# Kernel tuning notes

Measured on AMD Instinct MI355X. Metric: run time of the kernel, lower is better.

## Reference

```python
import jax, jax.numpy as jnp
import numpy as np

HIDDEN = 1024
NUM_HEADS = 16
HEAD_DIM = HIDDEN // NUM_HEADS


def setup_inputs() -> dict:
    key = jax.random.key(0)
    ks = jax.random.split(key, 9)
    B, S, Hs = 2, 2048, HIDDEN
    scale = 1.0 / np.sqrt(Hs)
    inp = {
        "hidden_state": jax.random.normal(ks[0], (B, S, Hs), dtype=jnp.float32),
        # causal mask, exactly (B, num_heads, S, S) as the module's assert requires
        "attention_mask": jnp.broadcast_to(
            jnp.tril(jnp.ones((S, S), dtype=bool)), (B, NUM_HEADS, S, S)
        ),
        "wq": jax.random.normal(ks[1], (Hs, Hs), dtype=jnp.float32) * scale,
        "bq": jnp.zeros((Hs,), dtype=jnp.float32),
        "wk": jax.random.normal(ks[2], (Hs, Hs), dtype=jnp.float32) * scale,
        "bk": jnp.zeros((Hs,), dtype=jnp.float32),
        "wv": jax.random.normal(ks[3], (Hs, Hs), dtype=jnp.float32) * scale,
        "bv": jnp.zeros((Hs,), dtype=jnp.float32),
        "wo": jax.random.normal(ks[4], (Hs, Hs), dtype=jnp.float32) * scale,
        "bo": jnp.zeros((Hs,), dtype=jnp.float32),
    }
    return inp


def _split_heads(x):
    B, S, _ = x.shape
    return x.reshape(B, S, NUM_HEADS, HEAD_DIM).transpose(0, 2, 1, 3)  # (B,H,S,D)


def reference(hidden_state, attention_mask, wq, bq, wk, bk, wv, bv, wo, bo):
    B, S, Hs = hidden_state.shape
    # torch nn.Linear: x @ W.T + b
    q = _split_heads(hidden_state @ wq.T + bq)
    k = _split_heads(hidden_state @ wk.T + bk)
    v = _split_heads(hidden_state @ wv.T + bv)
    scores = jnp.einsum("bhsd,bhtd->bhst", q, k) / jnp.sqrt(
        jnp.asarray(HEAD_DIM, dtype=jnp.float32)
    )
    scores = jnp.where(attention_mask, scores, -jnp.inf)
    probs = jax.nn.softmax(scores, axis=-1)
    # dropout p=0.0 (eval/deterministic) -> identity
    out = jnp.einsum("bhst,bhtd->bhsd", probs, v)
    out = out.transpose(0, 2, 1, 3).reshape(B, S, Hs)
    return out @ wo.T + bo
```

## Files before the change

kernel.cpp:

```cpp
#include <hip/hip_runtime.h>
#include <stdint.h>
#include <stddef.h>


typedef __attribute__((ext_vector_type(8))) short short8;
typedef __attribute__((ext_vector_type(4))) float f32x4;
typedef __attribute__((ext_vector_type(4))) unsigned int u32x4;
typedef __attribute__((ext_vector_type(4))) unsigned short u16x4;

static __device__ __forceinline__ unsigned short f2bf(float f){
  union { float f; unsigned u; } v; v.f = f;
  unsigned r = v.u + 0x7FFFu + ((v.u >> 16) & 1u);
  return (unsigned short)(r >> 16);
}

static __device__ __forceinline__ void gl_lds16(const void* g, void* l){
  __builtin_amdgcn_global_load_lds((const __attribute__((address_space(1))) void*)g,
                                   (__attribute__((address_space(3))) void*)l, 16, 0, 0);
}

__global__ __launch_bounds__(256) void k_cvt_all(const float* __restrict__ X,
                                                 const float* __restrict__ w0, const float* __restrict__ w1,
                                                 const float* __restrict__ w2, const float* __restrict__ w3,
                                                 unsigned short* __restrict__ Xb,
                                                 unsigned short* __restrict__ Wb){
  int bid = blockIdx.x;
  const float* src; unsigned short* dst; int i;
  if (bid < 4096){ src = X; dst = Xb; i = bid*256 + threadIdx.x; }
  else {
    int w = (bid - 4096) >> 10;
    const float* srcs[4] = {w0,w1,w2,w3};
    src = srcs[w]; dst = Wb + (size_t)w*1048576u;
    i = ((bid - 4096) & 1023)*256 + threadIdx.x;
  }
  f32x4 x = ((const f32x4*)src)[i];
  u16x4 y = { f2bf(x[0]), f2bf(x[1]), f2bf(x[2]), f2bf(x[3]) };
  ((u16x4*)dst)[i] = y;
}

template<int MODE>
__global__ __launch_bounds__(256) void k_gemm_bt(
    const unsigned short* __restrict__ A,
    const unsigned short* __restrict__ B,
    const float* __restrict__ bias0, const float* __restrict__ bias1, const float* __restrict__ bias2,
    void* __restrict__ Cout, int N, int K)
{
  __shared__ unsigned short lds_a[128*32];
  __shared__ unsigned short lds_b[128*32];
  const int t = threadIdx.x;
  const int lane = t & 63, wave = t >> 6;
  const int wy = wave >> 1, wx = wave & 1;
  const int m0 = blockIdx.y * 128, n0 = blockIdx.x * 128;
  const int mrow = lane & 15, quad = lane >> 4;
  const unsigned short* ga = A + (size_t)(m0 + (t>>2)) * K + (t&3)*8;
  const unsigned short* gb = B + (size_t)(n0 + (t>>2)) * K + (t&3)*8;
  char* la = (char*)lds_a + wave*1024;
  char* lb = (char*)lds_b + wave*1024;

  f32x4 acc[4][4];
  #pragma unroll
  for (int i=0;i<4;i++)
    #pragma unroll
    for (int j=0;j<4;j++) acc[i][j] = (f32x4){0.f,0.f,0.f,0.f};

  for (int k0=0;k0<K;k0+=32){
    __syncthreads();
    #pragma unroll
    for (int p=0;p<2;p++){
      gl_lds16(ga + (size_t)p*64*K + k0, la + p*4096);
      gl_lds16(gb + (size_t)p*64*K + k0, lb + p*4096);
    }
    __syncthreads();
    short8 af[4], bf[4];
    #pragma unroll
    for (int i=0;i<4;i++) af[i] = *(const short8*)(lds_a + (wy*64+i*16+mrow)*32 + quad*8);
    #pragma unroll
    for (int j=0;j<4;j++) bf[j] = *(const short8*)(lds_b + (wx*64+j*16+mrow)*32 + quad*8);
    #pragma unroll
    for (int i=0;i<4;i++)
      #pragma unroll
      for (int j=0;j<4;j++)
        acc[i][j] = __builtin_amdgcn_mfma_f32_16x16x32_bf16(af[i], bf[j], acc[i][j], 0,0,0);
  }

  #pragma unroll
  for (int j=0;j<4;j++){
    int col = n0 + wx*64 + j*16 + mrow;
    float bv;
    if (MODE==0){
      int cb = col >> 10;
      const float* bp = (cb==0)?bias0:((cb==1)?bias1:bias2);
      bv = bp[col & 1023];
    } else {
      bv = bias0[col];
    }
    #pragma unroll
    for (int i=0;i<4;i++){
      int rbase = m0 + wy*64 + i*16 + quad*4;
      #pragma unroll
      for (int r=0;r<4;r++){
        float v = acc[i][j][r] + bv;
        if (MODE==1) ((float*)Cout)[(size_t)(rbase+r)*N + col] = v;
        else         ((unsigned short*)Cout)[(size_t)(rbase+r)*N + col] = f2bf(v);
      }
    }
  }
}

__global__ __launch_bounds__(256) void k_vt(const unsigned short* __restrict__ QKV,
                                            unsigned short* __restrict__ Vt){
  __shared__ unsigned short tile[64][72];
  const int bh = blockIdx.y, b = bh >> 4, h = bh & 15;
  const int s0 = blockIdx.x * 64;
  const unsigned short* vp = QKV + (size_t)b*2048*3072 + 2048 + (size_t)h*64;
  const int r = threadIdx.x >> 3, c = (threadIdx.x & 7) * 8;
  #pragma unroll
  for (int p=0;p<2;p++){
    int s = r + p*32;
    *(u32x4*)&tile[s][c] = *(const u32x4*)(vp + (size_t)(s0+s)*3072 + c);
  }
  __syncthreads();
  unsigned short* op = Vt + (size_t)bh*64*2048;
  #pragma unroll
  for (int p=0;p<2;p++){
    int d = r + p*32;
    union { short8 v; unsigned short u[8]; } o;
    #pragma unroll
    for (int i=0;i<8;i++) o.u[i] = tile[c+i][d];
    *(short8*)(op + (size_t)d*2048 + s0 + c) = o.v;
  }
}

__global__ __launch_bounds__(256) void k_attn(const unsigned short* __restrict__ QKV,
                                              const unsigned short* __restrict__ Vt,
                                              unsigned short* __restrict__ Ctx){
  __shared__ unsigned short lds_k[64*72];
  __shared__ unsigned short lds_v[64*72];
  __shared__ unsigned short lds_p[4][16*72];
  const int t = threadIdx.x;
  const int lane = t & 63, wave = t >> 6;
  const int mrow = lane & 15, quad = lane >> 4;
  const int bh = blockIdx.y, b = bh >> 4, h = bh & 15;
  const int q0 = blockIdx.x * 64;
  const size_t qkvbase = (size_t)b*2048*3072 + (size_t)h*64;

  short8 qf[2];
  {
    const unsigned short* qp = QKV + qkvbase + (size_t)(q0 + wave*16 + mrow) * 3072;
    qf[0] = *(const short8*)(qp + quad*8);
    qf[1] = *(const short8*)(qp + 32 + quad*8);
  }
  float m_i[4], l_i[4]; f32x4 oacc[4];
  #pragma unroll
  for (int r=0;r<4;r++){ m_i[r] = -1e30f; l_i[r] = 0.f; }
  #pragma unroll
  for (int c=0;c<4;c++) oacc[c] = (f32x4){0.f,0.f,0.f,0.f};

  const int grow0 = q0 + wave*16 + quad*4;
  const int njt = blockIdx.x + 1;
  const unsigned short* kbase = QKV + qkvbase + 1024;
  const unsigned short* vbase = Vt + (size_t)bh*64*2048;
  const int sr = t >> 3, sc = (t & 7) * 8;

  for (int jt=0;jt<njt;jt++){
    const int j0 = jt*64;
    __syncthreads();
    #pragma unroll
    for (int p=0;p<2;p++){
      int r = sr + p*32;
      *(u32x4*)(lds_k + r*72 + sc) = *(const u32x4*)(kbase + (size_t)(j0+r)*3072 + sc);
      *(u32x4*)(lds_v + r*72 + sc) = *(const u32x4*)(vbase + (size_t)r*2048 + j0 + sc);
    }
    __syncthreads();

    f32x4 sacc[4];
    #pragma unroll
    for (int jj=0;jj<4;jj++) sacc[jj] = (f32x4){0.f,0.f,0.f,0.f};
    #pragma unroll
    for (int jj=0;jj<4;jj++)
      #pragma unroll
      for (int kk=0;kk<2;kk++){
        short8 kf = *(const short8*)(lds_k + (jj*16+mrow)*72 + kk*32 + quad*8);
        sacc[jj] = __builtin_amdgcn_mfma_f32_16x16x32_bf16(qf[kk], kf, sacc[jj], 0,0,0);
      }

    float s[4][4];
    if (jt == njt-1){
      #pragma unroll
      for (int jj=0;jj<4;jj++){
        int gcol = j0 + jj*16 + mrow;
        #pragma unroll
        for (int r=0;r<4;r++){
          float v = sacc[jj][r] * 0.125f;
          s[jj][r] = (gcol <= grow0 + r) ? v : -1e30f;
        }
      }
    } else {
      #pragma unroll
      for (int jj=0;jj<4;jj++)
        #pragma unroll
        for (int r=0;r<4;r++) s[jj][r] = sacc[jj][r] * 0.125f;
    }

    float alpha[4];
    #pragma unroll
    for (int r=0;r<4;r++){
      float v = fmaxf(fmaxf(s[0][r],s[1][r]), fmaxf(s[2][r],s[3][r]));
      #pragma unroll
      for (int off=1;off<16;off<<=1) v = fmaxf(v, __shfl_xor(v, off));
      float mn = fmaxf(m_i[r], v);
      alpha[r] = __expf(m_i[r] - mn);
      m_i[r] = mn;
    }
    #pragma unroll
    for (int r=0;r<4;r++){
      float sum = 0.f;
      #pragma unroll
      for (int jj=0;jj<4;jj++){
        float p = __expf(s[jj][r] - m_i[r]);
        s[jj][r] = p; sum += p;
      }
      #pragma unroll
      for (int off=1;off<16;off<<=1) sum += __shfl_xor(sum, off);
      l_i[r] = l_i[r]*alpha[r] + sum;
    }
    #pragma unroll
    for (int c=0;c<4;c++)
      #pragma unroll
      for (int r=0;r<4;r++) oacc[c][r] *= alpha[r];

    unsigned short* pp = lds_p[wave];
    #pragma unroll
    for (int jj=0;jj<4;jj++)
      #pragma unroll
      for (int r=0;r<4;r++)
        pp[(quad*4+r)*72 + jj*16 + mrow] = f2bf(s[jj][r]);
    __asm__ volatile("s_waitcnt lgkmcnt(0)" ::: "memory");
    short8 pf[2];
    pf[0] = *(const short8*)(pp + mrow*72 + quad*8);
    pf[1] = *(const short8*)(pp + mrow*72 + 32 + quad*8);

    #pragma unroll
    for (int c=0;c<4;c++)
      #pragma unroll
      for (int kk=0;kk<2;kk++){
        short8 vf = *(const short8*)(lds_v + (c*16+mrow)*72 + kk*32 + quad*8);
        oacc[c] = __builtin_amdgcn_mfma_f32_16x16x32_bf16(pf[kk], vf, oacc[c], 0,0,0);
      }
  }

  unsigned short* cp = Ctx + (size_t)b*2048*1024 + (size_t)h*64;
  #pragma unroll
  for (int c=0;c<4;c++)
    #pragma unroll
    for (int r=0;r<4;r++){
      float v = oacc[c][r] / l_i[r];
      cp[(size_t)(q0 + wave*16 + quad*4 + r)*1024 + c*16 + mrow] = f2bf(v);
    }
}

extern "C" void kernel_launch(void* const* d_in, const int* in_sizes, int n_in,
                              void* d_out, int out_size, void* d_ws, size_t ws_size,
                              hipStream_t stream){
  const float* X  = (const float*)d_in[0];
  const float* wq = (const float*)d_in[2];
  const float* bq = (const float*)d_in[3];
  const float* wk = (const float*)d_in[4];
  const float* bk = (const float*)d_in[5];
  const float* wv = (const float*)d_in[6];
  const float* bv = (const float*)d_in[7];
  const float* wo = (const float*)d_in[8];
  const float* bo = (const float*)d_in[9];

  char* ws = (char*)d_ws;
  unsigned short* Xb   = (unsigned short*)(ws);
  unsigned short* Wb   = (unsigned short*)(ws + (8u<<20));
  unsigned short* QKVb = (unsigned short*)(ws + (16u<<20));
  unsigned short* Vt   = (unsigned short*)(ws + (40u<<20));
  unsigned short* Ctxb = (unsigned short*)(ws + (48u<<20));

  k_cvt_all<<<dim3(8192), 256, 0, stream>>>(X, wq, wk, wv, wo, Xb, Wb);
  k_gemm_bt<0><<<dim3(24, 32), 256, 0, stream>>>(Xb, Wb, bq, bk, bv, QKVb, 3072, 1024);
  k_vt  <<<dim3(32, 32), 256, 0, stream>>>(QKVb, Vt);
  k_attn<<<dim3(32, 32), 256, 0, stream>>>(QKVb, Vt, Ctxb);
  k_gemm_bt<1><<<dim3(8, 32), 256, 0, stream>>>(Ctxb, Wb + 3u*1048576u, bo, bo, bo,
                                                d_out, 1024, 1024);
}
```

Measured before the change: 795.3 us.

## Process two query tiles per attention block and use 64-row tiles for output GEMM

The attention kernel now handles 128 query rows per block as two 64-row halves that share each loaded K/V tile. This halves K/V global traffic per query, and the first half skips the final diagonal tile. The output projection GEMM gets a 64-row M-tile variant with twice as many blocks, to fill more CUs on the small 1024-wide GEMM. The cost is fewer attention blocks (512), more registers per thread, and possible load imbalance from the causal triangle.

```diff
diff --git a/kernel.cpp b/kernel.cpp
--- a/kernel.cpp
+++ b/kernel.cpp
@@ -38,46 +38,48 @@
   ((u16x4*)dst)[i] = y;
 }
 
-template<int MODE>
+template<int MODE, int MT>
 __global__ __launch_bounds__(256) void k_gemm_bt(
     const unsigned short* __restrict__ A,
     const unsigned short* __restrict__ B,
     const float* __restrict__ bias0, const float* __restrict__ bias1, const float* __restrict__ bias2,
     void* __restrict__ Cout, int N, int K)
 {
-  __shared__ unsigned short lds_a[128*32];
+  static_assert(MT==64 || MT==128, "MT");
+  constexpr int I  = MT/32;
+  constexpr int NA = MT/64;
+  __shared__ unsigned short lds_a[MT*32];
   __shared__ unsigned short lds_b[128*32];
   const int t = threadIdx.x;
   const int lane = t & 63, wave = t >> 6;
   const int wy = wave >> 1, wx = wave & 1;
-  const int m0 = blockIdx.y * 128, n0 = blockIdx.x * 128;
+  const int m0 = blockIdx.y * MT, n0 = blockIdx.x * 128;
   const int mrow = lane & 15, quad = lane >> 4;
   const unsigned short* ga = A + (size_t)(m0 + (t>>2)) * K + (t&3)*8;
   const unsigned short* gb = B + (size_t)(n0 + (t>>2)) * K + (t&3)*8;
   char* la = (char*)lds_a + wave*1024;
   char* lb = (char*)lds_b + wave*1024;
 
-  f32x4 acc[4][4];
-  #pragma unroll
-  for (int i=0;i<4;i++)
+  f32x4 acc[I][4];
+  #pragma unroll
+  for (int i=0;i<I;i++)
     #pragma unroll
     for (int j=0;j<4;j++) acc[i][j] = (f32x4){0.f,0.f,0.f,0.f};
 
   for (int k0=0;k0<K;k0+=32){
     __syncthreads();
     #pragma unroll
-    for (int p=0;p<2;p++){
-      gl_lds16(ga + (size_t)p*64*K + k0, la + p*4096);
-      gl_lds16(gb + (size_t)p*64*K + k0, lb + p*4096);
-    }
+    for (int p=0;p<NA;p++) gl_lds16(ga + (size_t)p*64*K + k0, la + p*4096);
+    #pragma unroll
+    for (int p=0;p<2;p++)  gl_lds16(gb + (size_t)p*64*K + k0, lb + p*4096);
     __syncthreads();
-    short8 af[4], bf[4];
-    #pragma unroll
-    for (int i=0;i<4;i++) af[i] = *(const short8*)(lds_a + (wy*64+i*16+mrow)*32 + quad*8);
+    short8 af[I], bf[4];
+    #pragma unroll
+    for (int i=0;i<I;i++) af[i] = *(const short8*)(lds_a + (wy*(MT/2)+i*16+mrow)*32 + quad*8);
     #pragma unroll
     for (int j=0;j<4;j++) bf[j] = *(const short8*)(lds_b + (wx*64+j*16+mrow)*32 + quad*8);
     #pragma unroll
-    for (int i=0;i<4;i++)
+    for (int i=0;i<I;i++)
       #pragma unroll
       for (int j=0;j<4;j++)
         acc[i][j] = __builtin_amdgcn_mfma_f32_16x16x32_bf16(af[i], bf[j], acc[i][j], 0,0,0);
@@ -95,8 +97,8 @@
       bv = bias0[col];
     }
     #pragma unroll
-    for (int i=0;i<4;i++){
-      int rbase = m0 + wy*64 + i*16 + quad*4;
+    for (int i=0;i<I;i++){
+      int rbase = m0 + wy*(MT/2) + i*16 + quad*4;
       #pragma unroll
       for (int r=0;r<4;r++){
         float v = acc[i][j][r] + bv;
@@ -141,23 +143,26 @@
   const int lane = t & 63, wave = t >> 6;
   const int mrow = lane & 15, quad = lane >> 4;
   const int bh = blockIdx.y, b = bh >> 4, h = bh & 15;
-  const int q0 = blockIdx.x * 64;
+  const int q0 = blockIdx.x * 128;
   const size_t qkvbase = (size_t)b*2048*3072 + (size_t)h*64;
 
-  short8 qf[2];
-  {
-    const unsigned short* qp = QKV + qkvbase + (size_t)(q0 + wave*16 + mrow) * 3072;
-    qf[0] = *(const short8*)(qp + quad*8);
-    qf[1] = *(const short8*)(qp + 32 + quad*8);
-  }
-  float m_i[4], l_i[4]; f32x4 oacc[4];
-  #pragma unroll
-  for (int r=0;r<4;r++){ m_i[r] = -1e30f; l_i[r] = 0.f; }
-  #pragma unroll
-  for (int c=0;c<4;c++) oacc[c] = (f32x4){0.f,0.f,0.f,0.f};
-
-  const int grow0 = q0 + wave*16 + quad*4;
-  const int njt = blockIdx.x + 1;
+  short8 qf[2][2];
+  #pragma unroll
+  for (int qh=0;qh<2;qh++){
+    const unsigned short* qp = QKV + qkvbase + (size_t)(q0 + qh*64 + wave*16 + mrow) * 3072;
+    qf[qh][0] = *(const short8*)(qp + quad*8);
+    qf[qh][1] = *(const short8*)(qp + 32 + quad*8);
+  }
+  float m_i[2][4], l_i[2][4]; f32x4 oacc[2][4];
+  #pragma unroll
+  for (int qh=0;qh<2;qh++){
+    #pragma unroll
+    for (int r=0;r<4;r++){ m_i[qh][r] = -1e30f; l_i[qh][r] = 0.f; }
+    #pragma unroll
+    for (int c=0;c<4;c++) oacc[qh][c] = (f32x4){0.f,0.f,0.f,0.f};
+  }
+
+  const int njt = 2*blockIdx.x + 2;
   const unsigned short* kbase = QKV + qkvbase + 1024;
   const unsigned short* vbase = Vt + (size_t)bh*64*2048;
   const int sr = t >> 3, sc = (t & 7) * 8;
@@ -173,90 +178,98 @@
     }
     __syncthreads();
 
-    f32x4 sacc[4];
-    #pragma unroll
-    for (int jj=0;jj<4;jj++) sacc[jj] = (f32x4){0.f,0.f,0.f,0.f};
-    #pragma unroll
-    for (int jj=0;jj<4;jj++)
-      #pragma unroll
-      for (int kk=0;kk<2;kk++){
-        short8 kf = *(const short8*)(lds_k + (jj*16+mrow)*72 + kk*32 + quad*8);
-        sacc[jj] = __builtin_amdgcn_mfma_f32_16x16x32_bf16(qf[kk], kf, sacc[jj], 0,0,0);
-      }
-
-    float s[4][4];
-    if (jt == njt-1){
-      #pragma unroll
-      for (int jj=0;jj<4;jj++){
-        int gcol = j0 + jj*16 + mrow;
-        #pragma unroll
-        for (int r=0;r<4;r++){
-          float v = sacc[jj][r] * 0.125f;
-          s[jj][r] = (gcol <= grow0 + r) ? v : -1e30f;
+    #pragma unroll
+    for (int qh=0;qh<2;qh++){
+      if (qh==0 && jt==njt-1) continue;
+      const int grow0 = q0 + qh*64 + wave*16 + quad*4;
+
+      f32x4 sacc[4];
+      #pragma unroll
+      for (int jj=0;jj<4;jj++) sacc[jj] = (f32x4){0.f,0.f,0.f,0.f};
+      #pragma unroll
+      for (int jj=0;jj<4;jj++)
+        #pragma unroll
+        for (int kk=0;kk<2;kk++){
+          short8 kf = *(const short8*)(lds_k + (jj*16+mrow)*72 + kk*32 + quad*8);
+          sacc[jj] = __builtin_amdgcn_mfma_f32_16x16x32_bf16(qf[qh][kk], kf, sacc[jj], 0,0,0);
         }
-      }
-    } else {
+
+      float s[4][4];
+      if (jt == 2*blockIdx.x + qh){
+        #pragma unroll
+        for (int jj=0;jj<4;jj++){
+          int gcol = j0 + jj*16 + mrow;
+          #pragma unroll
+          for (int r=0;r<4;r++){
+            float v = sacc[jj][r] * 0.125f;
+            s[jj][r] = (gcol <= grow0 + r) ? v : -1e30f;
+          }
+        }
+      } else {
+        #pragma unroll
+        for (int jj=0;jj<4;jj++)
+          #pragma unroll
+          for (int r=0;r<4;r++) s[jj][r] = sacc[jj][r] * 0.125f;
+      }
+
+      float alpha[4];
+      #pragma unroll
+      for (int r=0;r<4;r++){
+        float v = fmaxf(fmaxf(s[0][r],s[1][r]), fmaxf(s[2][r],s[3][r]));
+        #pragma unroll
+        for (int off=1;off<16;off<<=1) v = fmaxf(v, __shfl_xor(v, off));
+        float mn = fmaxf(m_i[qh][r], v);
+        alpha[r] = __expf(m_i[qh][r] - mn);
+        m_i[qh][r] = mn;
+      }
+      #pragma unroll
+      for (int r=0;r<4;r++){
+        float sum = 0.f;
+        #pragma unroll
+        for (int jj=0;jj<4;jj++){
+          float p = __expf(s[jj][r] - m_i[qh][r]);
+          s[jj][r] = p; sum += p;
+        }
+        #pragma unroll
+        for (int off=1;off<16;off<<=1) sum += __shfl_xor(sum, off);
+        l_i[qh][r] = l_i[qh][r]*alpha[r] + sum;
+      }
+      #pragma unroll
+      for (int c=0;c<4;c++)
+        #pragma unroll
+        for (int r=0;r<4;r++) oacc[qh][c][r] *= alpha[r];
+
+      unsigned short* pp = lds_p[wave];
       #pragma unroll
       for (int jj=0;jj<4;jj++)
         #pragma unroll
-        for (int r=0;r<4;r++) s[jj][r] = sacc[jj][r] * 0.125f;
+        for (int r=0;r<4;r++)
+          pp[(quad*4+r)*72 + jj*16 + mrow] = f2bf(s[jj][r]);
+      __asm__ volatile("s_waitcnt lgkmcnt(0)" ::: "memory");
+      short8 pf[2];
+      pf[0] = *(const short8*)(pp + mrow*72 + quad*8);
+      pf[1] = *(const short8*)(pp + mrow*72 + 32 + quad*8);
+
+      #pragma unroll
+      for (int c=0;c<4;c++)
+        #pragma unroll
+        for (int kk=0;kk<2;kk++){
+          short8 vf = *(const short8*)(lds_v + (c*16+mrow)*72 + kk*32 + quad*8);
+          oacc[qh][c] = __builtin_amdgcn_mfma_f32_16x16x32_bf16(pf[kk], vf, oacc[qh][c], 0,0,0);
+        }
     }
-
-    float alpha[4];
-    #pragma unroll
-    for (int r=0;r<4;r++){
-      float v = fmaxf(fmaxf(s[0][r],s[1][r]), fmaxf(s[2][r],s[3][r]));
-      #pragma unroll
-      for (int off=1;off<16;off<<=1) v = fmaxf(v, __shfl_xor(v, off));
-      float mn = fmaxf(m_i[r], v);
-      alpha[r] = __expf(m_i[r] - mn);
-      m_i[r] = mn;
-    }
-    #pragma unroll
-    for (int r=0;r<4;r++){
-      float sum = 0.f;
-      #pragma unroll
-      for (int jj=0;jj<4;jj++){
-        float p = __expf(s[jj][r] - m_i[r]);
-        s[jj][r] = p; sum += p;
-      }
-      #pragma unroll
-      for (int off=1;off<16;off<<=1) sum += __shfl_xor(sum, off);
-      l_i[r] = l_i[r]*alpha[r] + sum;
-    }
+  }
+
+  unsigned short* cp = Ctx + (size_t)b*2048*1024 + (size_t)h*64;
+  #pragma unroll
+  for (int qh=0;qh<2;qh++)
     #pragma unroll
     for (int c=0;c<4;c++)
       #pragma unroll
-      for (int r=0;r<4;r++) oacc[c][r] *= alpha[r];
-
-    unsigned short* pp = lds_p[wave];
-    #pragma unroll
-    for (int jj=0;jj<4;jj++)
-      #pragma unroll
-      for (int r=0;r<4;r++)
-        pp[(quad*4+r)*72 + jj*16 + mrow] = f2bf(s[jj][r]);
-    __asm__ volatile("s_waitcnt lgkmcnt(0)" ::: "memory");
-    short8 pf[2];
-    pf[0] = *(const short8*)(pp + mrow*72 + quad*8);
-    pf[1] = *(const short8*)(pp + mrow*72 + 32 + quad*8);
-
-    #pragma unroll
-    for (int c=0;c<4;c++)
-      #pragma unroll
-      for (int kk=0;kk<2;kk++){
-        short8 vf = *(const short8*)(lds_v + (c*16+mrow)*72 + kk*32 + quad*8);
-        oacc[c] = __builtin_amdgcn_mfma_f32_16x16x32_bf16(pf[kk], vf, oacc[c], 0,0,0);
-      }
-  }
-
-  unsigned short* cp = Ctx + (size_t)b*2048*1024 + (size_t)h*64;
-  #pragma unroll
-  for (int c=0;c<4;c++)
-    #pragma unroll
-    for (int r=0;r<4;r++){
-      float v = oacc[c][r] / l_i[r];
-      cp[(size_t)(q0 + wave*16 + quad*4 + r)*1024 + c*16 + mrow] = f2bf(v);
-    }
+      for (int r=0;r<4;r++){
+        float v = oacc[qh][c][r] / l_i[qh][r];
+        cp[(size_t)(q0 + qh*64 + wave*16 + quad*4 + r)*1024 + c*16 + mrow] = f2bf(v);
+      }
 }
 
 extern "C" void kernel_launch(void* const* d_in, const int* in_sizes, int n_in,
@@ -280,9 +293,9 @@
   unsigned short* Ctxb = (unsigned short*)(ws + (48u<<20));
 
   k_cvt_all<<<dim3(8192), 256, 0, stream>>>(X, wq, wk, wv, wo, Xb, Wb);
-  k_gemm_bt<0><<<dim3(24, 32), 256, 0, stream>>>(Xb, Wb, bq, bk, bv, QKVb, 3072, 1024);
+  k_gemm_bt<0,128><<<dim3(24, 32), 256, 0, stream>>>(Xb, Wb, bq, bk, bv, QKVb, 3072, 1024);
   k_vt  <<<dim3(32, 32), 256, 0, stream>>>(QKVb, Vt);
-  k_attn<<<dim3(32, 32), 256, 0, stream>>>(QKVb, Vt, Ctxb);
-  k_gemm_bt<1><<<dim3(8, 32), 256, 0, stream>>>(Ctxb, Wb + 3u*1048576u, bo, bo, bo,
-                                                d_out, 1024, 1024);
-}
+  k_attn<<<dim3(16, 32), 256, 0, stream>>>(QKVb, Vt, Ctxb);
+  k_gemm_bt<1,64><<<dim3(8, 64), 256, 0, stream>>>(Ctxb, Wb + 3u*1048576u, bo, bo, bo,
+                                                   d_out, 1024, 1024);
+}
```

New measurement: 775.2 us. -2.5%, faster.
